# Kernel tuning notes

Measured on AMD Instinct MI355X. Metric: run time of the kernel, lower is better.

The kernel has to match this reference:

```python
import jax, jax.numpy as jnp
import numpy as np

N_GRAPHS = 32
NUM_NODES = 2848
N = N_GRAPHS * NUM_NODES  # 91136
E = 1_000_000
K = 3   # num_stacks
T = 5   # num_layers
HID = 32
EPS = 1e-5


def setup_inputs() -> dict:
    key = jax.random.key(0)
    ks = jax.random.split(key, 32)
    s = 0.1
    rn = lambda k, shp: (jax.random.normal(k, shp, jnp.float32) * s)
    inp = {
        "x": jax.random.normal(ks[0], (N, 2), jnp.float32),
        "edge_index": jax.random.randint(ks[1], (2, E), 0, N, dtype=jnp.int32).astype(jnp.int64),
        "weights": jax.random.uniform(ks[2], (E,), jnp.float32),
        "batch": (jnp.arange(N) // NUM_NODES).astype(jnp.int64),
        # ARMAConv1: 2 -> 32
        "iw1": rn(ks[3], (K, 2, HID)),
        "w1": rn(ks[4], (T - 1, K, HID, HID)),
        "rw1": rn(ks[5], (T, K, 2, HID)),
        "b1": rn(ks[6], (T, K, 1, HID)),
        "g1": jnp.ones((HID,), jnp.float32), "be1": jnp.zeros((HID,), jnp.float32),
        # ARMAConv2: 32 -> 32
        "iw2": rn(ks[7], (K, HID, HID)),
        "w2": rn(ks[8], (T - 1, K, HID, HID)),
        "rw2": rn(ks[9], (T, K, HID, HID)),
        "b2": rn(ks[10], (T, K, 1, HID)),
        "g2": jnp.ones((HID,), jnp.float32), "be2": jnp.zeros((HID,), jnp.float32),
        # ARMAConv3: 32 -> 1
        "iw3": rn(ks[11], (K, HID, 1)),
        "w3": rn(ks[12], (T - 1, K, 1, 1)),
        "rw3": rn(ks[13], (T, K, HID, 1)),
        "b3": rn(ks[14], (T, K, 1, 1)),
        "g3": jnp.ones((1,), jnp.float32), "be3": jnp.zeros((1,), jnp.float32),
        # classifier Linear(1, 1)
        "cw": rn(ks[15], (1, 1)),
        "cb": jnp.zeros((1,), jnp.float32),
    }
    return inp


def gcn_norm(row, col, w, n):
    # deg over targets, sym normalization, no self loops (PyG ARMAConv default)
    deg = jnp.zeros((n,), w.dtype).at[col].add(w)
    dis = jnp.where(deg > 0, jax.lax.rsqrt(jnp.where(deg > 0, deg, 1.0)), 0.0)
    return dis[row] * w * dis[col]


def arma_conv(x, row, col, norm, iw, w, rw, b):
    # x: [N, Fin]; returns [N, Fout] (mean over K stacks)
    out = None
    for t in range(T):
        if t == 0:
            h = jnp.einsum('nf,kfo->kno', x, iw)          # [K, N, Fout]
        else:
            h = jnp.einsum('kno,kop->knp', out, w[t - 1])
        msg = h[:, row, :] * norm[None, :, None]           # [K, E, Fout]
        agg = jnp.zeros_like(h).at[:, col, :].add(msg)     # scatter to targets
        out = jax.nn.relu(agg + jnp.einsum('nf,kfo->kno', x, rw[t]) + b[t])
    return out.mean(axis=0)


def batch_norm(x, g, b):
    m = x.mean(axis=0)
    v = x.var(axis=0)  # biased, as torch BatchNorm1d (training stats)
    return (x - m) * jax.lax.rsqrt(v + EPS) * g + b


def reference(x, edge_index, weights, batch,
              iw1, w1, rw1, b1, g1, be1,
              iw2, w2, rw2, b2, g2, be2,
              iw3, w3, rw3, b3, g3, be3,
              cw, cb):
    row, col = edge_index[0], edge_index[1]
    norm = gcn_norm(row, col, weights, N)

    h = arma_conv(x, row, col, norm, iw1, w1, rw1, b1)
    h = jax.nn.relu(batch_norm(h, g1, be1))
    h = arma_conv(h, row, col, norm, iw2, w2, rw2, b2)
    h = jax.nn.relu(batch_norm(h, g2, be2))
    h = arma_conv(h, row, col, norm, iw3, w3, rw3, b3)
    h = jax.nn.relu(batch_norm(h, g3, be3))  # [N, 1]

    # to_dense_batch: each graph has exactly NUM_NODES nodes -> reshape
    xd = h.reshape(N_GRAPHS, NUM_NODES, 1)
    logits_nodes = (xd @ cw.T + cb).squeeze(-1)   # [B, NUM_NODES]
    logits_graph = logits_nodes.max(axis=1)       # [B]
    return logits_nodes, logits_graph
```

## Files before the change

kernel.cpp:

```cpp
#include <hip/hip_runtime.h>
#include <hip/hip_fp16.h>

#define N_GRAPHS 32
#define NUM_NODES 2848
#define NTOT (N_GRAPHS * NUM_NODES)
#define NE 1000000
#define KS 3
#define TL 5
#define HID 32
#define EPSV 1e-5f
#define SCAN_B 256
#define NBLK (NTOT / SCAN_B)
#define NBINS 64
#define CNTN (NBINS * NBLK)
#define CNTB (CNTN / SCAN_B)
#define NT8 (NTOT * 8)
#define NB128 (NTOT / 128)
#define SRCMASK 0x1FFFFu

typedef unsigned uintx4 __attribute__((ext_vector_type(4)));


__device__ __forceinline__ float2 unpk(unsigned u) {
    return make_float2(__uint_as_float(u << 16), __uint_as_float(u & 0xffff0000u));
}
__device__ __forceinline__ unsigned bf16rn(float f) {
    unsigned x = __float_as_uint(f);
    return (x + 0x7fffu + ((x >> 16) & 1u)) >> 16;
}
__device__ __forceinline__ unsigned pk(float a, float b) {
    return bf16rn(a) | (bf16rn(b) << 16);
}
__device__ __forceinline__ float dec_nm(unsigned q) {
    return __half2float(__ushort_as_half((unsigned short)(q >> 17)));
}


__global__ void k_cnt(const int* __restrict__ col, int* __restrict__ indeg) {
    int e = blockIdx.x * blockDim.x + threadIdx.x;
    if (e < NE) atomicAdd(&indeg[col[e]], 1);
}

__global__ void k_lhist(const int* __restrict__ indeg, int* __restrict__ cnt) {
    __shared__ int h[NBINS];
    int t = threadIdx.x;
    if (t < NBINS) h[t] = 0;
    __syncthreads();
    int n = blockIdx.x * SCAN_B + t;
    atomicAdd(&h[min(indeg[n], NBINS - 1)], 1);
    __syncthreads();
    if (t < NBINS) cnt[t * NBLK + blockIdx.x] = h[t];
}

__global__ void k_scan1(const int* __restrict__ in, int* __restrict__ bsum) {
    __shared__ int s[SCAN_B];
    int i = blockIdx.x * SCAN_B + threadIdx.x;
    s[threadIdx.x] = in[i];
    __syncthreads();
    for (int st = SCAN_B / 2; st >= 1; st >>= 1) {
        if (threadIdx.x < st) s[threadIdx.x] += s[threadIdx.x + st];
        __syncthreads();
    }
    if (threadIdx.x == 0) bsum[blockIdx.x] = s[0];
}

__global__ void k_scan2(int* __restrict__ bsum, int n) {
    __shared__ int s[512];
    int t = threadIdx.x;
    int v = (t < n) ? bsum[t] : 0;
    s[t] = v;
    __syncthreads();
    for (int off = 1; off < 512; off <<= 1) {
        int a = (t >= off) ? s[t - off] : 0;
        __syncthreads();
        s[t] += a;
        __syncthreads();
    }
    if (t < n) bsum[t] = s[t] - v;
}

__global__ void k_scan3(const int* __restrict__ in, const int* __restrict__ bsum,
                        int* __restrict__ out, int sentIdx, int sentVal) {
    __shared__ int s[SCAN_B];
    int i = blockIdx.x * SCAN_B + threadIdx.x;
    int v = in[i];
    s[threadIdx.x] = v;
    __syncthreads();
    for (int off = 1; off < SCAN_B; off <<= 1) {
        int a = (threadIdx.x >= off) ? s[threadIdx.x - off] : 0;
        __syncthreads();
        s[threadIdx.x] += a;
        __syncthreads();
    }
    out[i] = bsum[blockIdx.x] + s[threadIdx.x] - v;
    if (i == 0 && sentIdx >= 0) out[sentIdx] = sentVal;
}

__global__ void k_rank(const int* __restrict__ indeg, const int* __restrict__ cnt,
                       int* __restrict__ perm, int* __restrict__ invperm,
                       int* __restrict__ indegp) {
    __shared__ int base[NBINS];
    __shared__ int cur[NBINS];
    int t = threadIdx.x;
    if (t < NBINS) { base[t] = cnt[t * NBLK + blockIdx.x]; cur[t] = 0; }
    __syncthreads();
    int n = blockIdx.x * SCAN_B + t;
    int dg = indeg[n];
    int b = min(dg, NBINS - 1);
    int pos = base[b] + atomicAdd(&cur[b], 1);
    perm[pos] = n;
    invperm[n] = pos;
    indegp[pos] = dg;
}

__global__ void k_xp(const float2* __restrict__ x, const int* __restrict__ perm,
                     float2* __restrict__ xp) {
    int i = blockIdx.x * blockDim.x + threadIdx.x;
    if (i < NTOT) xp[i] = x[perm[i]];
}

__global__ void k_fill(const int* __restrict__ row, const int* __restrict__ col,
                       const float* __restrict__ w, const int* __restrict__ invperm,
                       int* __restrict__ cursor, int2* __restrict__ adjtmp) {
    int e = blockIdx.x * blockDim.x + threadIdx.x;
    if (e < NE) {
        int pr = invperm[row[e]], pc = invperm[col[e]];
        int p = atomicAdd(&cursor[pc], 1);
        adjtmp[p] = make_int2(pr, __float_as_int(w[e]));
    }
}

__global__ void k_degdis(const int2* __restrict__ adjtmp, const int* __restrict__ offs,
                         float* __restrict__ disp) {
    int n = blockIdx.x * blockDim.x + threadIdx.x;
    if (n >= NTOT) return;
    int e0 = offs[n], e1 = offs[n + 1];
    float d = 0.f;
    for (int e = e0; e < e1; ++e) d += __int_as_float(adjtmp[e].y);
    disp[n] = (d > 0.f) ? rsqrtf(d) : 0.f;
}

__global__ void k_norm(const int2* __restrict__ adjtmp, const int* __restrict__ offs,
                       const float* __restrict__ disp, unsigned* __restrict__ adjc) {
    int n = blockIdx.x * blockDim.x + threadIdx.x;
    if (n >= NTOT) return;
    float dc = disp[n];
    int e0 = offs[n], e1 = offs[n + 1];
    for (int e = e0; e < e1; ++e) {
        int2 t = adjtmp[e];
        float nm = dc * __int_as_float(t.y) * disp[t.x];
        unsigned short hb = __half_as_ushort(__float2half(nm));
        adjc[e] = ((unsigned)hb << 17) | (unsigned)t.x;
    }
}


__global__ __launch_bounds__(256) void k_gath(
    const unsigned* __restrict__ SRC, const int* __restrict__ offs,
    const unsigned* __restrict__ adjc, unsigned* __restrict__ P) {
    int tid = threadIdx.x;
    int u = tid & 1;
    int nl = tid >> 1;
    int bid = blockIdx.x;
    int s = bid / NB128;
    int node = (bid - s * NB128) * 128 + nl;
    const uintx4* src = (const uintx4*)(SRC + (size_t)s * NT8);
    float a0 = 0.f, a1 = 0.f, a2 = 0.f, a3 = 0.f, a4 = 0.f, a5 = 0.f, a6 = 0.f, a7 = 0.f;
    int e0 = offs[node], e1 = offs[node + 1];
    int e = e0;
    for (; e + 4 <= e1; e += 4) {
        unsigned q0 = __builtin_nontemporal_load(adjc + e);
        unsigned q1 = __builtin_nontemporal_load(adjc + e + 1);
        unsigned q2 = __builtin_nontemporal_load(adjc + e + 2);
        unsigned q3 = __builtin_nontemporal_load(adjc + e + 3);
        uintx4 v0 = src[(q0 & SRCMASK) * 2 + u];
        uintx4 v1 = src[(q1 & SRCMASK) * 2 + u];
        uintx4 v2 = src[(q2 & SRCMASK) * 2 + u];
        uintx4 v3 = src[(q3 & SRCMASK) * 2 + u];
        float n0 = dec_nm(q0), n1 = dec_nm(q1), n2 = dec_nm(q2), n3 = dec_nm(q3);
        float2 t;
        t = unpk(v0.x); a0 += n0 * t.x; a1 += n0 * t.y;
        t = unpk(v0.y); a2 += n0 * t.x; a3 += n0 * t.y;
        t = unpk(v0.z); a4 += n0 * t.x; a5 += n0 * t.y;
        t = unpk(v0.w); a6 += n0 * t.x; a7 += n0 * t.y;
        t = unpk(v1.x); a0 += n1 * t.x; a1 += n1 * t.y;
        t = unpk(v1.y); a2 += n1 * t.x; a3 += n1 * t.y;
        t = unpk(v1.z); a4 += n1 * t.x; a5 += n1 * t.y;
        t = unpk(v1.w); a6 += n1 * t.x; a7 += n1 * t.y;
        t = unpk(v2.x); a0 += n2 * t.x; a1 += n2 * t.y;
        t = unpk(v2.y); a2 += n2 * t.x; a3 += n2 * t.y;
        t = unpk(v2.z); a4 += n2 * t.x; a5 += n2 * t.y;
        t = unpk(v2.w); a6 += n2 * t.x; a7 += n2 * t.y;
        t = unpk(v3.x); a0 += n3 * t.x; a1 += n3 * t.y;
        t = unpk(v3.y); a2 += n3 * t.x; a3 += n3 * t.y;
        t = unpk(v3.z); a4 += n3 * t.x; a5 += n3 * t.y;
        t = unpk(v3.w); a6 += n3 * t.x; a7 += n3 * t.y;
    }
    for (; e < e1; ++e) {
        unsigned q0 = __builtin_nontemporal_load(adjc + e);
        uintx4 v0 = src[(q0 & SRCMASK) * 2 + u];
        float n0 = dec_nm(q0);
        float2 t;
        t = unpk(v0.x); a0 += n0 * t.x; a1 += n0 * t.y;
        t = unpk(v0.y); a2 += n0 * t.x; a3 += n0 * t.y;
        t = unpk(v0.z); a4 += n0 * t.x; a5 += n0 * t.y;
        t = unpk(v0.w); a6 += n0 * t.x; a7 += n0 * t.y;
    }
    uintx4 o;
    o.x = pk(a0, a1); o.y = pk(a2, a3); o.z = pk(a4, a5); o.w = pk(a6, a7);
    __builtin_nontemporal_store(o, (uintx4*)(P + (size_t)s * NT8 + (size_t)node * 8) + u);
}


template<int FIN, bool PERK, bool LAST>
__global__ __launch_bounds__(256) void k_xform(
    const unsigned* __restrict__ P, const float* __restrict__ xin,
    const float* __restrict__ W, const float* __restrict__ rw,
    const float* __restrict__ bb, unsigned* __restrict__ OUTn,
    float* __restrict__ xm) {
    constexpr int SPK = PERK ? 3 : 1;
    constexpr int NSEC = PERK ? 6 : 2;
    constexpr int ND = 128;
    __shared__ unsigned sp[SPK][ND][17];
    __shared__ float xr[FIN == 32 ? ND : 1][FIN == 32 ? 33 : 1];
    int tid = threadIdx.x;
    int node0 = blockIdx.x * ND;
    for (int t4 = tid; t4 < NSEC * 256; t4 += 256) {
        int s = t4 >> 8, r = t4 & 255, n = r >> 1, u4 = (r & 1) * 4;
        uintx4 v = *(const uintx4*)(P + (size_t)s * NT8 + (size_t)(node0 + n) * 8 + u4);
        int kk = PERK ? (s >> 1) : 0;
        int base = (s & 1) * 8 + u4;
        sp[kk][n][base]     = v.x;
        sp[kk][n][base + 1] = v.y;
        sp[kk][n][base + 2] = v.z;
        sp[kk][n][base + 3] = v.w;
    }
    if constexpr (FIN == 32) {
        for (int t4 = tid; t4 < ND * 8; t4 += 256) {
            int n = t4 >> 3, j4 = (t4 & 7) * 4;
            float4 v = ((const float4*)xin)[(size_t)(node0 + n) * 8 + (t4 & 7)];
            xr[n][j4] = v.x; xr[n][j4 + 1] = v.y; xr[n][j4 + 2] = v.z; xr[n][j4 + 3] = v.w;
        }
    }
    __syncthreads();
    int f2 = tid & 15, nl = tid >> 4;
    int nbase = nl * 8;
    float2 xv2[8];
    if constexpr (FIN == 2) {
#pragma unroll
        for (int n = 0; n < 8; ++n) xv2[n] = ((const float2*)xin)[node0 + nbase + n];
    }
    float m0[8] = {}, m1[8] = {};
#pragma unroll
    for (int k = 0; k < KS; ++k) {
        constexpr int kkI = 0;
        const int kk = PERK ? k : kkI;
        float2 bv = ((const float2*)(bb + k * HID))[f2];
        float h0[8], h1[8];
#pragma unroll
        for (int n = 0; n < 8; ++n) { h0[n] = bv.x; h1[n] = bv.y; }
        const float2* W2 = (const float2*)(W + (size_t)k * HID * HID);
        const float2* R2 = (const float2*)(rw + (size_t)k * FIN * HID);
#pragma unroll 4
        for (int i2 = 0; i2 < 16; ++i2) {
            float2 wf0 = W2[(2 * i2) * 16 + f2];
            float2 wf1 = W2[(2 * i2 + 1) * 16 + f2];
            float2 rf0, rf1;
            if constexpr (FIN == 32) {
                rf0 = R2[(2 * i2) * 16 + f2];
                rf1 = R2[(2 * i2 + 1) * 16 + f2];
            }
#pragma unroll
            for (int n = 0; n < 8; ++n) {
                float2 sv = unpk(sp[kk][nbase + n][i2]);
                h0[n] += sv.x * wf0.x + sv.y * wf1.x;
                h1[n] += sv.x * wf0.y + sv.y * wf1.y;
                if constexpr (FIN == 32) {
                    float x0 = xr[nbase + n][2 * i2], x1 = xr[nbase + n][2 * i2 + 1];
                    h0[n] += x0 * rf0.x + x1 * rf1.x;
                    h1[n] += x0 * rf0.y + x1 * rf1.y;
                }
            }
        }
        if constexpr (FIN == 2) {
            float2 r0 = R2[0 * 16 + f2], r1 = R2[1 * 16 + f2];
#pragma unroll
            for (int n = 0; n < 8; ++n) {
                h0[n] += xv2[n].x * r0.x + xv2[n].y * r1.x;
                h1[n] += xv2[n].x * r0.y + xv2[n].y * r1.y;
            }
        }
#pragma unroll
        for (int n = 0; n < 8; ++n) {
            h0[n] = fmaxf(h0[n], 0.f);
            h1[n] = fmaxf(h1[n], 0.f);
            if constexpr (LAST) {
                m0[n] += h0[n]; m1[n] += h1[n];
            } else {
                OUTn[(size_t)(k * 2 + (f2 >> 3)) * NT8 +
                     (size_t)(node0 + nbase + n) * 8 + (f2 & 7)] = pk(h0[n], h1[n]);
            }
        }
    }
    if constexpr (LAST) {
#pragma unroll
        for (int n = 0; n < 8; ++n)
            ((float2*)xm)[(size_t)(node0 + nbase + n) * 16 + f2] =
                make_float2(m0[n] * (1.f / 3.f), m1[n] * (1.f / 3.f));
    }
}


__global__ void k_gath2(const float2* __restrict__ xp, const int* __restrict__ offs,
                        const unsigned* __restrict__ adjc, float2* __restrict__ pag) {
    int node = blockIdx.x * blockDim.x + threadIdx.x;
    if (node >= NTOT) return;
    float a0 = 0.f, a1 = 0.f;
    int e0 = offs[node], e1 = offs[node + 1];
    int e = e0;
    for (; e + 4 <= e1; e += 4) {
        unsigned q0 = __builtin_nontemporal_load(adjc + e);
        unsigned q1 = __builtin_nontemporal_load(adjc + e + 1);
        unsigned q2 = __builtin_nontemporal_load(adjc + e + 2);
        unsigned q3 = __builtin_nontemporal_load(adjc + e + 3);
        float2 x0 = xp[q0 & SRCMASK], x1 = xp[q1 & SRCMASK];
        float2 x2 = xp[q2 & SRCMASK], x3 = xp[q3 & SRCMASK];
        float n0 = dec_nm(q0), n1 = dec_nm(q1), n2 = dec_nm(q2), n3 = dec_nm(q3);
        a0 += n0 * x0.x + n1 * x1.x + n2 * x2.x + n3 * x3.x;
        a1 += n0 * x0.y + n1 * x1.y + n2 * x2.y + n3 * x3.y;
    }
    for (; e < e1; ++e) {
        unsigned q0 = __builtin_nontemporal_load(adjc + e);
        float2 xs = xp[q0 & SRCMASK];
        float nm = dec_nm(q0);
        a0 += nm * xs.x; a1 += nm * xs.y;
    }
    pag[node] = make_float2(a0, a1);
}

__global__ void k_x0(const float2* __restrict__ pag, const float2* __restrict__ xp,
                     const float* __restrict__ iw, const float* __restrict__ rw0,
                     const float* __restrict__ b0, unsigned* __restrict__ OUT) {
    int tid = blockIdx.x * blockDim.x + threadIdx.x;
    int f2 = tid & 15;
    int node = tid >> 4;
    float2 pv = pag[node];
    float2 xn = xp[node];
#pragma unroll
    for (int k = 0; k < KS; ++k) {
        const float2* iw2 = (const float2*)(iw + k * 2 * HID);
        const float2* rw2 = (const float2*)(rw0 + k * 2 * HID);
        float2 wi0 = iw2[0 * 16 + f2], wi1 = iw2[1 * 16 + f2];
        float2 wr0 = rw2[0 * 16 + f2], wr1 = rw2[1 * 16 + f2];
        float2 bv = ((const float2*)(b0 + k * HID))[f2];
        float o0 = fmaxf(pv.x * wi0.x + pv.y * wi1.x + xn.x * wr0.x + xn.y * wr1.x + bv.x, 0.f);
        float o1 = fmaxf(pv.x * wi0.y + pv.y * wi1.y + xn.x * wr0.y + xn.y * wr1.y + bv.y, 0.f);
        OUT[(size_t)(k * 2 + (f2 >> 3)) * NT8 + (size_t)node * 8 + (f2 & 7)] = pk(o0, o1);
    }
}


__global__ void k_init1(const float* __restrict__ x, const float* __restrict__ iw,
                        float4* __restrict__ H) {
    int n = blockIdx.x * blockDim.x + threadIdx.x;
    if (n >= NTOT) return;
    float a0 = 0.f, a1 = 0.f, a2 = 0.f;
#pragma unroll
    for (int i = 0; i < HID; ++i) {
        float xv = x[n * HID + i];
        a0 += xv * iw[0 * HID + i];
        a1 += xv * iw[1 * HID + i];
        a2 += xv * iw[2 * HID + i];
    }
    H[n] = make_float4(a0, a1, a2, 0.f);
}

template<bool LAST>
__global__ void k_prop1(const float4* __restrict__ H, const float* __restrict__ xin,
                        const float* __restrict__ rw_t, const float* __restrict__ b_t,
                        const float* __restrict__ W_t, const int* __restrict__ offs,
                        const unsigned* __restrict__ adjc, const int* __restrict__ perm,
                        float* __restrict__ outp) {
    int node = blockIdx.x * blockDim.x + threadIdx.x;
    if (node >= NTOT) return;
    float a0 = b_t[0], a1 = b_t[1], a2 = b_t[2];
#pragma unroll
    for (int i = 0; i < HID; ++i) {
        float xv = xin[node * HID + i];
        a0 += xv * rw_t[0 * HID + i];
        a1 += xv * rw_t[1 * HID + i];
        a2 += xv * rw_t[2 * HID + i];
    }
    int e0 = offs[node], e1 = offs[node + 1];
    int e = e0;
    for (; e + 4 <= e1; e += 4) {
        unsigned q0 = __builtin_nontemporal_load(adjc + e);
        unsigned q1 = __builtin_nontemporal_load(adjc + e + 1);
        unsigned q2 = __builtin_nontemporal_load(adjc + e + 2);
        unsigned q3 = __builtin_nontemporal_load(adjc + e + 3);
        float4 h0 = H[q0 & SRCMASK], h1 = H[q1 & SRCMASK];
        float4 h2 = H[q2 & SRCMASK], h3 = H[q3 & SRCMASK];
        float n0 = dec_nm(q0), n1 = dec_nm(q1), n2 = dec_nm(q2), n3 = dec_nm(q3);
        a0 += n0 * h0.x; a1 += n0 * h0.y; a2 += n0 * h0.z;
        a0 += n1 * h1.x; a1 += n1 * h1.y; a2 += n1 * h1.z;
        a0 += n2 * h2.x; a1 += n2 * h2.y; a2 += n2 * h2.z;
        a0 += n3 * h3.x; a1 += n3 * h3.y; a2 += n3 * h3.z;
    }
    for (; e < e1; ++e) {
        unsigned q0 = __builtin_nontemporal_load(adjc + e);
        float4 h = H[q0 & SRCMASK];
        float nm = dec_nm(q0);
        a0 += nm * h.x; a1 += nm * h.y; a2 += nm * h.z;
    }
    a0 = fmaxf(a0, 0.f); a1 = fmaxf(a1, 0.f); a2 = fmaxf(a2, 0.f);
    if constexpr (LAST) {
        outp[perm[node]] = (a0 + a1 + a2) * (1.f / 3.f);
    } else {
        ((float4*)outp)[node] = make_float4(a0 * W_t[0], a1 * W_t[1], a2 * W_t[2], 0.f);
    }
}


__global__ void k_bnstats(const float* __restrict__ x, float* __restrict__ stats, int F) {
    __shared__ float s1[256];
    __shared__ float s2[256];
    int tid = threadIdx.x;
    int gid = blockIdx.x * blockDim.x + tid;
    int stride = gridDim.x * blockDim.x;
    int total = NTOT * F;
    float a = 0.f, b = 0.f;
    for (int i = gid; i < total; i += stride) {
        float v = x[i];
        a += v;
        b += v * v;
    }
    s1[tid] = a; s2[tid] = b;
    __syncthreads();
    for (int s = 128; s >= F; s >>= 1) {
        if (tid < s) { s1[tid] += s1[tid + s]; s2[tid] += s2[tid + s]; }
        __syncthreads();
    }
    if (tid < F) {
        atomicAdd(&stats[tid], s1[tid]);
        atomicAdd(&stats[F + tid], s2[tid]);
    }
}

__global__ void k_bnapply32(float* __restrict__ x, const float* __restrict__ stats,
                            const float* __restrict__ g, const float* __restrict__ be,
                            unsigned* __restrict__ xbf) {
    int tid = blockIdx.x * blockDim.x + threadIdx.x;
    int f2 = tid & 15;
    int node = tid >> 4;
    int f0 = 2 * f2, f1 = f0 + 1;
    float mm0 = stats[f0] * (1.f / NTOT);
    float vv0 = stats[HID + f0] * (1.f / NTOT) - mm0 * mm0;
    float mm1 = stats[f1] * (1.f / NTOT);
    float vv1 = stats[HID + f1] * (1.f / NTOT) - mm1 * mm1;
    float y0 = fmaxf((x[(size_t)node * 32 + f0] - mm0) * rsqrtf(vv0 + EPSV) * g[f0] + be[f0], 0.f);
    float y1 = fmaxf((x[(size_t)node * 32 + f1] - mm1) * rsqrtf(vv1 + EPSV) * g[f1] + be[f1], 0.f);
    x[(size_t)node * 32 + f0] = y0;
    x[(size_t)node * 32 + f1] = y1;
    if (xbf) xbf[(size_t)(f2 >> 3) * NT8 + (size_t)node * 8 + (f2 & 7)] = pk(y0, y1);
}

__global__ void k_bnapply1(float* __restrict__ x, const float* __restrict__ stats,
                           const float* __restrict__ g, const float* __restrict__ be) {
    int i = blockIdx.x * blockDim.x + threadIdx.x;
    if (i >= NTOT) return;
    float m = stats[0] * (1.f / NTOT);
    float v = stats[1] * (1.f / NTOT) - m * m;
    float y = (x[i] - m) * rsqrtf(v + EPSV) * g[0] + be[0];
    x[i] = fmaxf(y, 0.f);
}


__global__ void k_final(const float* __restrict__ h, const float* __restrict__ cw,
                        const float* __restrict__ cb, float* __restrict__ out) {
    __shared__ float smax[256];
    int g = blockIdx.x;
    float cwv = cw[0], cbv = cb[0];
    float mx = -INFINITY;
    for (int i = threadIdx.x; i < NUM_NODES; i += blockDim.x) {
        int nidx = g * NUM_NODES + i;
        float v = h[nidx] * cwv + cbv;
        out[nidx] = v;
        mx = fmaxf(mx, v);
    }
    smax[threadIdx.x] = mx;
    __syncthreads();
    for (int s = 128; s >= 1; s >>= 1) {
        if (threadIdx.x < s) smax[threadIdx.x] = fmaxf(smax[threadIdx.x], smax[threadIdx.x + s]);
        __syncthreads();
    }
    if (threadIdx.x == 0) out[NTOT + g] = smax[0];
}


extern "C" void kernel_launch(void* const* d_in, const int* in_sizes, int n_in,
                              void* d_out, int out_size, void* d_ws, size_t ws_size,
                              hipStream_t stream) {
    const float* x   = (const float*)d_in[0];
    const int*   ei  = (const int*)d_in[1];
    const int*   row = ei;
    const int*   col = ei + NE;
    const float* wts = (const float*)d_in[2];
    const float* iw1 = (const float*)d_in[4];
    const float* w1  = (const float*)d_in[5];
    const float* rw1 = (const float*)d_in[6];
    const float* b1  = (const float*)d_in[7];
    const float* g1  = (const float*)d_in[8];
    const float* be1 = (const float*)d_in[9];
    const float* iw2 = (const float*)d_in[10];
    const float* w2  = (const float*)d_in[11];
    const float* rw2 = (const float*)d_in[12];
    const float* b2  = (const float*)d_in[13];
    const float* g2  = (const float*)d_in[14];
    const float* be2 = (const float*)d_in[15];
    const float* iw3 = (const float*)d_in[16];
    const float* w3  = (const float*)d_in[17];
    const float* rw3 = (const float*)d_in[18];
    const float* b3  = (const float*)d_in[19];
    const float* g3  = (const float*)d_in[20];
    const float* be3 = (const float*)d_in[21];
    const float* cw  = (const float*)d_in[22];
    const float* cb  = (const float*)d_in[23];
    float* out = (float*)d_out;

    char* p = (char*)d_ws;
    auto alloc = [&](size_t bytes) {
        char* r = p;
        p += (bytes + 255) & ~(size_t)255;
        return r;
    };
    int*      indeg  = (int*)alloc((size_t)NTOT * 4);
    int*      cnt    = (int*)alloc((size_t)CNTN * 4);
    char*     zend   = p;
    int*      bsum   = (int*)alloc((size_t)NBLK * 4);
    int*      offs   = (int*)alloc((size_t)(NTOT + 1) * 4);
    int*      cursor = (int*)alloc((size_t)NTOT * 4);
    int*      perm   = (int*)alloc((size_t)NTOT * 4);
    int*      invperm= (int*)alloc((size_t)NTOT * 4);
    int*      indegp = (int*)alloc((size_t)NTOT * 4);
    float*    disp   = (float*)alloc((size_t)NTOT * 4);
    int2*     adjtmp = (int2*)alloc((size_t)NE * 8);
    unsigned* adjc   = (unsigned*)alloc((size_t)NE * 4);
    unsigned* OUTA   = (unsigned*)alloc((size_t)6 * NT8 * 4);
    unsigned* OUTB   = (unsigned*)alloc((size_t)6 * NT8 * 4);
    unsigned* P      = (unsigned*)alloc((size_t)6 * NT8 * 4);
    unsigned* xplane = (unsigned*)alloc((size_t)2 * NT8 * 4);
    float2*   xp     = (float2*)alloc((size_t)NTOT * 8);
    float2*   pag    = (float2*)alloc((size_t)NTOT * 8);
    float*    xa     = (float*)alloc((size_t)NTOT * HID * 4);
    float*    xb     = (float*)alloc((size_t)NTOT * HID * 4);
    float*    xc     = (float*)alloc((size_t)NTOT * 4);
    float*    stats  = (float*)alloc(3 * 2 * HID * 4);
    if ((size_t)(p - (char*)d_ws) > ws_size) return;

    const int tb = 256;
    const int ebl = (NE + tb - 1) / tb;
    const int nbl = NTOT / tb;
    const int g16 = NTOT * 16 / tb;

    hipMemsetAsync(indeg, 0, (size_t)(zend - (char*)indeg), stream);
    hipMemsetAsync(stats, 0, (size_t)3 * 2 * HID * 4, stream);

    k_cnt<<<ebl, tb, 0, stream>>>(col, indeg);
    k_lhist<<<NBLK, SCAN_B, 0, stream>>>(indeg, cnt);
    k_scan1<<<CNTB, SCAN_B, 0, stream>>>(cnt, bsum);
    k_scan2<<<1, 512, 0, stream>>>(bsum, CNTB);
    k_scan3<<<CNTB, SCAN_B, 0, stream>>>(cnt, bsum, cnt, -1, 0);
    k_rank<<<NBLK, SCAN_B, 0, stream>>>(indeg, cnt, perm, invperm, indegp);
    k_xp<<<nbl, tb, 0, stream>>>((const float2*)x, perm, xp);
    k_scan1<<<NBLK, SCAN_B, 0, stream>>>(indegp, bsum);
    k_scan2<<<1, 512, 0, stream>>>(bsum, NBLK);
    k_scan3<<<NBLK, SCAN_B, 0, stream>>>(indegp, bsum, offs, NTOT, NE);
    hipMemcpyAsync(cursor, offs, (size_t)NTOT * 4, hipMemcpyDeviceToDevice, stream);
    k_fill<<<ebl, tb, 0, stream>>>(row, col, wts, invperm, cursor, adjtmp);
    k_degdis<<<nbl, tb, 0, stream>>>(adjtmp, offs, disp);
    k_norm<<<nbl, tb, 0, stream>>>(adjtmp, offs, disp, adjc);

    {
        k_gath2<<<nbl, tb, 0, stream>>>(xp, offs, adjc, pag);
        k_x0<<<g16, tb, 0, stream>>>(pag, xp, iw1, rw1, b1, OUTA);
        unsigned* Hc = OUTA; unsigned* Hn = OUTB;
        for (int t = 1; t < TL - 1; ++t) {
            k_gath<<<6 * NB128, tb, 0, stream>>>(Hc, offs, adjc, P);
            k_xform<2, true, false><<<NB128, tb, 0, stream>>>(
                P, (const float*)xp, w1 + (size_t)(t - 1) * KS * HID * HID,
                rw1 + (size_t)t * KS * 2 * HID, b1 + (size_t)t * KS * HID, Hn, nullptr);
            unsigned* tmp = Hc; Hc = Hn; Hn = tmp;
        }
        k_gath<<<6 * NB128, tb, 0, stream>>>(Hc, offs, adjc, P);
        k_xform<2, true, true><<<NB128, tb, 0, stream>>>(
            P, (const float*)xp, w1 + (size_t)(TL - 2) * KS * HID * HID,
            rw1 + (size_t)(TL - 1) * KS * 2 * HID, b1 + (size_t)(TL - 1) * KS * HID,
            nullptr, xa);
        k_bnstats<<<256, tb, 0, stream>>>(xa, stats, HID);
        k_bnapply32<<<g16, tb, 0, stream>>>(xa, stats, g1, be1, xplane);
    }
    {
        k_gath<<<2 * NB128, tb, 0, stream>>>(xplane, offs, adjc, P);
        k_xform<32, false, false><<<NB128, tb, 0, stream>>>(
            P, xa, iw2, rw2, b2, OUTA, nullptr);
        unsigned* Hc = OUTA; unsigned* Hn = OUTB;
        for (int t = 1; t < TL - 1; ++t) {
            k_gath<<<6 * NB128, tb, 0, stream>>>(Hc, offs, adjc, P);
            k_xform<32, true, false><<<NB128, tb, 0, stream>>>(
                P, xa, w2 + (size_t)(t - 1) * KS * HID * HID,
                rw2 + (size_t)t * KS * HID * HID, b2 + (size_t)t * KS * HID, Hn, nullptr);
            unsigned* tmp = Hc; Hc = Hn; Hn = tmp;
        }
        k_gath<<<6 * NB128, tb, 0, stream>>>(Hc, offs, adjc, P);
        k_xform<32, true, true><<<NB128, tb, 0, stream>>>(
            P, xa, w2 + (size_t)(TL - 2) * KS * HID * HID,
            rw2 + (size_t)(TL - 1) * KS * HID * HID, b2 + (size_t)(TL - 1) * KS * HID,
            nullptr, xb);
        k_bnstats<<<256, tb, 0, stream>>>(xb, stats + 2 * HID, HID);
        k_bnapply32<<<g16, tb, 0, stream>>>(xb, stats + 2 * HID, g2, be2, nullptr);
    }
    {
        float4* HAf = (float4*)OUTA;
        float4* HBf = (float4*)OUTB;
        k_init1<<<nbl, tb, 0, stream>>>(xb, iw3, HAf);
        const float4* Hc = HAf; float4* Hn = HBf;
        for (int t = 0; t < TL - 1; ++t) {
            k_prop1<false><<<nbl, tb, 0, stream>>>(
                Hc, xb, rw3 + (size_t)t * KS * HID, b3 + (size_t)t * KS,
                w3 + (size_t)t * KS, offs, adjc, perm, (float*)Hn);
            const float4* tmp = Hc; Hc = Hn; Hn = (float4*)tmp;
        }
        k_prop1<true><<<nbl, tb, 0, stream>>>(
            Hc, xb, rw3 + (size_t)(TL - 1) * KS * HID, b3 + (size_t)(TL - 1) * KS,
            nullptr, offs, adjc, perm, xc);
        k_bnstats<<<256, tb, 0, stream>>>(xc, stats + 4 * HID, 1);
        k_bnapply1<<<nbl, tb, 0, stream>>>(xc, stats + 4 * HID, g3, be3);
    }

    k_final<<<N_GRAPHS, 256, 0, stream>>>(xc, cw, cb, out);
}
```

Before: 1.171 ms.

## Make gather kernel persistent with XCC-affine atomic work queue per feature section

Replaces the one-block-per-(section, node chunk) gather launch with a fixed grid of persistent blocks. Each block pulls node chunks from per-section atomic counters, starting with a section chosen from its XCC id. The goal is for each XCC to work mostly on one source section so its gathered rows stay in that XCC's L2, cutting cross-die traffic and misses. The cost is an atomic plus two barriers per chunk, and XCC-to-section imbalance falls back to stealing from other sections. The counters are zeroed once per call by the existing memset and get a fresh slot for each launch.

```diff
diff --git a/kernel.cpp b/kernel.cpp
--- a/kernel.cpp
+++ b/kernel.cpp
@@ -17,6 +17,7 @@
 #define NT8 (NTOT * 8)
 #define NB128 (NTOT / 128)
 #define SRCMASK 0x1FFFFu
+#define QSLOTS 16
 
 typedef unsigned uintx4 __attribute__((ext_vector_type(4)));
 
@@ -157,58 +158,77 @@
 
 __global__ __launch_bounds__(256) void k_gath(
     const unsigned* __restrict__ SRC, const int* __restrict__ offs,
-    const unsigned* __restrict__ adjc, unsigned* __restrict__ P) {
+    const unsigned* __restrict__ adjc, unsigned* __restrict__ P,
+    int* __restrict__ qcur, int nsec) {
+    __shared__ int sc_s, sc_c;
+    unsigned xcc = 0;
+    asm volatile("s_getreg_b32 %0, hwreg(HW_REG_XCC_ID)" : "=s"(xcc));
+    int prim = (int)(xcc & 7) % nsec;
     int tid = threadIdx.x;
     int u = tid & 1;
     int nl = tid >> 1;
-    int bid = blockIdx.x;
-    int s = bid / NB128;
-    int node = (bid - s * NB128) * 128 + nl;
-    const uintx4* src = (const uintx4*)(SRC + (size_t)s * NT8);
-    float a0 = 0.f, a1 = 0.f, a2 = 0.f, a3 = 0.f, a4 = 0.f, a5 = 0.f, a6 = 0.f, a7 = 0.f;
-    int e0 = offs[node], e1 = offs[node + 1];
-    int e = e0;
-    for (; e + 4 <= e1; e += 4) {
-        unsigned q0 = __builtin_nontemporal_load(adjc + e);
-        unsigned q1 = __builtin_nontemporal_load(adjc + e + 1);
-        unsigned q2 = __builtin_nontemporal_load(adjc + e + 2);
-        unsigned q3 = __builtin_nontemporal_load(adjc + e + 3);
-        uintx4 v0 = src[(q0 & SRCMASK) * 2 + u];
-        uintx4 v1 = src[(q1 & SRCMASK) * 2 + u];
-        uintx4 v2 = src[(q2 & SRCMASK) * 2 + u];
-        uintx4 v3 = src[(q3 & SRCMASK) * 2 + u];
-        float n0 = dec_nm(q0), n1 = dec_nm(q1), n2 = dec_nm(q2), n3 = dec_nm(q3);
-        float2 t;
-        t = unpk(v0.x); a0 += n0 * t.x; a1 += n0 * t.y;
-        t = unpk(v0.y); a2 += n0 * t.x; a3 += n0 * t.y;
-        t = unpk(v0.z); a4 += n0 * t.x; a5 += n0 * t.y;
-        t = unpk(v0.w); a6 += n0 * t.x; a7 += n0 * t.y;
-        t = unpk(v1.x); a0 += n1 * t.x; a1 += n1 * t.y;
-        t = unpk(v1.y); a2 += n1 * t.x; a3 += n1 * t.y;
-        t = unpk(v1.z); a4 += n1 * t.x; a5 += n1 * t.y;
-        t = unpk(v1.w); a6 += n1 * t.x; a7 += n1 * t.y;
-        t = unpk(v2.x); a0 += n2 * t.x; a1 += n2 * t.y;
-        t = unpk(v2.y); a2 += n2 * t.x; a3 += n2 * t.y;
-        t = unpk(v2.z); a4 += n2 * t.x; a5 += n2 * t.y;
-        t = unpk(v2.w); a6 += n2 * t.x; a7 += n2 * t.y;
-        t = unpk(v3.x); a0 += n3 * t.x; a1 += n3 * t.y;
-        t = unpk(v3.y); a2 += n3 * t.x; a3 += n3 * t.y;
-        t = unpk(v3.z); a4 += n3 * t.x; a5 += n3 * t.y;
-        t = unpk(v3.w); a6 += n3 * t.x; a7 += n3 * t.y;
-    }
-    for (; e < e1; ++e) {
-        unsigned q0 = __builtin_nontemporal_load(adjc + e);
-        uintx4 v0 = src[(q0 & SRCMASK) * 2 + u];
-        float n0 = dec_nm(q0);
-        float2 t;
-        t = unpk(v0.x); a0 += n0 * t.x; a1 += n0 * t.y;
-        t = unpk(v0.y); a2 += n0 * t.x; a3 += n0 * t.y;
-        t = unpk(v0.z); a4 += n0 * t.x; a5 += n0 * t.y;
-        t = unpk(v0.w); a6 += n0 * t.x; a7 += n0 * t.y;
-    }
-    uintx4 o;
-    o.x = pk(a0, a1); o.y = pk(a2, a3); o.z = pk(a4, a5); o.w = pk(a6, a7);
-    __builtin_nontemporal_store(o, (uintx4*)(P + (size_t)s * NT8 + (size_t)node * 8) + u);
+    for (;;) {
+        if (tid == 0) {
+            int s = -1, c = -1;
+            for (int t = 0; t < nsec; ++t) {
+                int ss = prim + t; if (ss >= nsec) ss -= nsec;
+                int cc = atomicAdd(&qcur[ss], 1);
+                if (cc < NB128) { s = ss; c = cc; break; }
+            }
+            sc_s = s; sc_c = c;
+        }
+        __syncthreads();
+        int s = sc_s, c = sc_c;
+        __syncthreads();
+        if (s < 0) return;
+        int node = c * 128 + nl;
+        const uintx4* src = (const uintx4*)(SRC + (size_t)s * NT8);
+        float a0 = 0.f, a1 = 0.f, a2 = 0.f, a3 = 0.f;
+        float a4 = 0.f, a5 = 0.f, a6 = 0.f, a7 = 0.f;
+        int e0 = offs[node], e1 = offs[node + 1];
+        int e = e0;
+        for (; e + 4 <= e1; e += 4) {
+            unsigned q0 = __builtin_nontemporal_load(adjc + e);
+            unsigned q1 = __builtin_nontemporal_load(adjc + e + 1);
+            unsigned q2 = __builtin_nontemporal_load(adjc + e + 2);
+            unsigned q3 = __builtin_nontemporal_load(adjc + e + 3);
+            uintx4 v0 = src[(q0 & SRCMASK) * 2 + u];
+            uintx4 v1 = src[(q1 & SRCMASK) * 2 + u];
+            uintx4 v2 = src[(q2 & SRCMASK) * 2 + u];
+            uintx4 v3 = src[(q3 & SRCMASK) * 2 + u];
+            float n0 = dec_nm(q0), n1 = dec_nm(q1), n2 = dec_nm(q2), n3 = dec_nm(q3);
+            float2 t;
+            t = unpk(v0.x); a0 += n0 * t.x; a1 += n0 * t.y;
+            t = unpk(v0.y); a2 += n0 * t.x; a3 += n0 * t.y;
+            t = unpk(v0.z); a4 += n0 * t.x; a5 += n0 * t.y;
+            t = unpk(v0.w); a6 += n0 * t.x; a7 += n0 * t.y;
+            t = unpk(v1.x); a0 += n1 * t.x; a1 += n1 * t.y;
+            t = unpk(v1.y); a2 += n1 * t.x; a3 += n1 * t.y;
+            t = unpk(v1.z); a4 += n1 * t.x; a5 += n1 * t.y;
+            t = unpk(v1.w); a6 += n1 * t.x; a7 += n1 * t.y;
+            t = unpk(v2.x); a0 += n2 * t.x; a1 += n2 * t.y;
+            t = unpk(v2.y); a2 += n2 * t.x; a3 += n2 * t.y;
+            t = unpk(v2.z); a4 += n2 * t.x; a5 += n2 * t.y;
+            t = unpk(v2.w); a6 += n2 * t.x; a7 += n2 * t.y;
+            t = unpk(v3.x); a0 += n3 * t.x; a1 += n3 * t.y;
+            t = unpk(v3.y); a2 += n3 * t.x; a3 += n3 * t.y;
+            t = unpk(v3.z); a4 += n3 * t.x; a5 += n3 * t.y;
+            t = unpk(v3.w); a6 += n3 * t.x; a7 += n3 * t.y;
+        }
+        for (; e < e1; ++e) {
+            unsigned q0 = __builtin_nontemporal_load(adjc + e);
+            uintx4 v0 = src[(q0 & SRCMASK) * 2 + u];
+            float n0 = dec_nm(q0);
+            float2 t;
+            t = unpk(v0.x); a0 += n0 * t.x; a1 += n0 * t.y;
+            t = unpk(v0.y); a2 += n0 * t.x; a3 += n0 * t.y;
+            t = unpk(v0.z); a4 += n0 * t.x; a5 += n0 * t.y;
+            t = unpk(v0.w); a6 += n0 * t.x; a7 += n0 * t.y;
+        }
+        uintx4 o;
+        o.x = pk(a0, a1); o.y = pk(a2, a3); o.z = pk(a4, a5); o.w = pk(a6, a7);
+        __builtin_nontemporal_store(o, (uintx4*)(P + (size_t)s * NT8 + (size_t)node * 8) + u);
+    }
 }
 
 
@@ -535,6 +555,7 @@
     };
     int*      indeg  = (int*)alloc((size_t)NTOT * 4);
     int*      cnt    = (int*)alloc((size_t)CNTN * 4);
+    int*      qcur   = (int*)alloc((size_t)QSLOTS * 8 * 4);
     char*     zend   = p;
     int*      bsum   = (int*)alloc((size_t)NBLK * 4);
     int*      offs   = (int*)alloc((size_t)(NTOT + 1) * 4);
@@ -561,6 +582,8 @@
     const int ebl = (NE + tb - 1) / tb;
     const int nbl = NTOT / tb;
     const int g16 = NTOT * 16 / tb;
+    const int gpers = 2048;
+    int qslot = 0;
 
     hipMemsetAsync(indeg, 0, (size_t)(zend - (char*)indeg), stream);
     hipMemsetAsync(stats, 0, (size_t)3 * 2 * HID * 4, stream);
@@ -585,13 +608,13 @@
         k_x0<<<g16, tb, 0, stream>>>(pag, xp, iw1, rw1, b1, OUTA);
         unsigned* Hc = OUTA; unsigned* Hn = OUTB;
         for (int t = 1; t < TL - 1; ++t) {
-            k_gath<<<6 * NB128, tb, 0, stream>>>(Hc, offs, adjc, P);
+            k_gath<<<gpers, tb, 0, stream>>>(Hc, offs, adjc, P, qcur + 8 * qslot++, 6);
             k_xform<2, true, false><<<NB128, tb, 0, stream>>>(
                 P, (const float*)xp, w1 + (size_t)(t - 1) * KS * HID * HID,
                 rw1 + (size_t)t * KS * 2 * HID, b1 + (size_t)t * KS * HID, Hn, nullptr);
             unsigned* tmp = Hc; Hc = Hn; Hn = tmp;
         }
-        k_gath<<<6 * NB128, tb, 0, stream>>>(Hc, offs, adjc, P);
+        k_gath<<<gpers, tb, 0, stream>>>(Hc, offs, adjc, P, qcur + 8 * qslot++, 6);
         k_xform<2, true, true><<<NB128, tb, 0, stream>>>(
             P, (const float*)xp, w1 + (size_t)(TL - 2) * KS * HID * HID,
             rw1 + (size_t)(TL - 1) * KS * 2 * HID, b1 + (size_t)(TL - 1) * KS * HID,
@@ -600,18 +623,18 @@
         k_bnapply32<<<g16, tb, 0, stream>>>(xa, stats, g1, be1, xplane);
     }
     {
-        k_gath<<<2 * NB128, tb, 0, stream>>>(xplane, offs, adjc, P);
+        k_gath<<<gpers, tb, 0, stream>>>(xplane, offs, adjc, P, qcur + 8 * qslot++, 2);
         k_xform<32, false, false><<<NB128, tb, 0, stream>>>(
             P, xa, iw2, rw2, b2, OUTA, nullptr);
         unsigned* Hc = OUTA; unsigned* Hn = OUTB;
         for (int t = 1; t < TL - 1; ++t) {
-            k_gath<<<6 * NB128, tb, 0, stream>>>(Hc, offs, adjc, P);
+            k_gath<<<gpers, tb, 0, stream>>>(Hc, offs, adjc, P, qcur + 8 * qslot++, 6);
             k_xform<32, true, false><<<NB128, tb, 0, stream>>>(
                 P, xa, w2 + (size_t)(t - 1) * KS * HID * HID,
                 rw2 + (size_t)t * KS * HID * HID, b2 + (size_t)t * KS * HID, Hn, nullptr);
             unsigned* tmp = Hc; Hc = Hn; Hn = tmp;
         }
-        k_gath<<<6 * NB128, tb, 0, stream>>>(Hc, offs, adjc, P);
+        k_gath<<<gpers, tb, 0, stream>>>(Hc, offs, adjc, P, qcur + 8 * qslot++, 6);
         k_xform<32, true, true><<<NB128, tb, 0, stream>>>(
             P, xa, w2 + (size_t)(TL - 2) * KS * HID * HID,
             rw2 + (size_t)(TL - 1) * KS * HID * HID, b2 + (size_t)(TL - 1) * KS * HID,
```

Result: slower. 2.366 ms (+102.1%).

## Pack edge weights into compressed adjacency and precompute layer-3 root terms

Applied to the files above, without the earlier changes.

The edge fill now writes the 32-bit packed adjacency directly, storing the raw edge weight as fp16 alongside the source index, and the degree and normalization kernels read and rewrite that packed array in place instead of an 8-byte int2 temporary. In the third ARMA layer, a new kernel reads each node's 32-wide features once and computes the initial projection plus all five root-weight projections, storing them in a per-layer float4 buffer. The propagation kernels then load a single float4 instead of re-reading 32 floats per step. This trades fp16 rounding of the raw weights in the degree sum (a precision risk) and an extra buffer for less memory traffic.

```diff
diff --git a/kernel.cpp b/kernel.cpp
--- a/kernel.cpp
+++ b/kernel.cpp
@@ -121,36 +121,37 @@
 
 __global__ void k_fill(const int* __restrict__ row, const int* __restrict__ col,
                        const float* __restrict__ w, const int* __restrict__ invperm,
-                       int* __restrict__ cursor, int2* __restrict__ adjtmp) {
+                       int* __restrict__ cursor, unsigned* __restrict__ adjc) {
     int e = blockIdx.x * blockDim.x + threadIdx.x;
     if (e < NE) {
         int pr = invperm[row[e]], pc = invperm[col[e]];
         int p = atomicAdd(&cursor[pc], 1);
-        adjtmp[p] = make_int2(pr, __float_as_int(w[e]));
-    }
-}
-
-__global__ void k_degdis(const int2* __restrict__ adjtmp, const int* __restrict__ offs,
+        unsigned short hb = __half_as_ushort(__float2half(w[e]));
+        adjc[p] = ((unsigned)hb << 17) | (unsigned)pr;
+    }
+}
+
+__global__ void k_degdis(const unsigned* __restrict__ adjc, const int* __restrict__ offs,
                          float* __restrict__ disp) {
     int n = blockIdx.x * blockDim.x + threadIdx.x;
     if (n >= NTOT) return;
     int e0 = offs[n], e1 = offs[n + 1];
     float d = 0.f;
-    for (int e = e0; e < e1; ++e) d += __int_as_float(adjtmp[e].y);
+    for (int e = e0; e < e1; ++e) d += dec_nm(adjc[e]);
     disp[n] = (d > 0.f) ? rsqrtf(d) : 0.f;
 }
 
-__global__ void k_norm(const int2* __restrict__ adjtmp, const int* __restrict__ offs,
-                       const float* __restrict__ disp, unsigned* __restrict__ adjc) {
+__global__ void k_norm(unsigned* __restrict__ adjc, const int* __restrict__ offs,
+                       const float* __restrict__ disp) {
     int n = blockIdx.x * blockDim.x + threadIdx.x;
     if (n >= NTOT) return;
     float dc = disp[n];
     int e0 = offs[n], e1 = offs[n + 1];
     for (int e = e0; e < e1; ++e) {
-        int2 t = adjtmp[e];
-        float nm = dc * __int_as_float(t.y) * disp[t.x];
+        unsigned q = adjc[e];
+        float nm = dc * dec_nm(q) * disp[q & SRCMASK];
         unsigned short hb = __half_as_ushort(__float2half(nm));
-        adjc[e] = ((unsigned)hb << 17) | (unsigned)t.x;
+        adjc[e] = ((unsigned)hb << 17) | (q & SRCMASK);
     }
 }
 
@@ -360,37 +361,50 @@
 }
 
 
-__global__ void k_init1(const float* __restrict__ x, const float* __restrict__ iw,
-                        float4* __restrict__ H) {
+__global__ void k_rec3(const float* __restrict__ xb, const float* __restrict__ iw3,
+                       const float* __restrict__ rw3, const float* __restrict__ b3,
+                       float4* __restrict__ H0, float4* __restrict__ RT) {
     int n = blockIdx.x * blockDim.x + threadIdx.x;
     if (n >= NTOT) return;
-    float a0 = 0.f, a1 = 0.f, a2 = 0.f;
-#pragma unroll
-    for (int i = 0; i < HID; ++i) {
-        float xv = x[n * HID + i];
-        a0 += xv * iw[0 * HID + i];
-        a1 += xv * iw[1 * HID + i];
-        a2 += xv * iw[2 * HID + i];
-    }
-    H[n] = make_float4(a0, a1, a2, 0.f);
+    float xr[HID];
+#pragma unroll
+    for (int j = 0; j < 8; ++j) {
+        float4 v = ((const float4*)xb)[(size_t)n * 8 + j];
+        xr[4 * j] = v.x; xr[4 * j + 1] = v.y; xr[4 * j + 2] = v.z; xr[4 * j + 3] = v.w;
+    }
+    {
+        float a0 = 0.f, a1 = 0.f, a2 = 0.f;
+#pragma unroll
+        for (int i = 0; i < HID; ++i) {
+            a0 += xr[i] * iw3[0 * HID + i];
+            a1 += xr[i] * iw3[1 * HID + i];
+            a2 += xr[i] * iw3[2 * HID + i];
+        }
+        H0[n] = make_float4(a0, a1, a2, 0.f);
+    }
+#pragma unroll
+    for (int t = 0; t < TL; ++t) {
+        float a0 = b3[t * KS + 0], a1 = b3[t * KS + 1], a2 = b3[t * KS + 2];
+        const float* r = rw3 + (size_t)t * KS * HID;
+#pragma unroll
+        for (int i = 0; i < HID; ++i) {
+            a0 += xr[i] * r[0 * HID + i];
+            a1 += xr[i] * r[1 * HID + i];
+            a2 += xr[i] * r[2 * HID + i];
+        }
+        RT[(size_t)t * NTOT + n] = make_float4(a0, a1, a2, 0.f);
+    }
 }
 
 template<bool LAST>
-__global__ void k_prop1(const float4* __restrict__ H, const float* __restrict__ xin,
-                        const float* __restrict__ rw_t, const float* __restrict__ b_t,
+__global__ void k_prop1(const float4* __restrict__ H, const float4* __restrict__ RT,
                         const float* __restrict__ W_t, const int* __restrict__ offs,
                         const unsigned* __restrict__ adjc, const int* __restrict__ perm,
                         float* __restrict__ outp) {
     int node = blockIdx.x * blockDim.x + threadIdx.x;
     if (node >= NTOT) return;
-    float a0 = b_t[0], a1 = b_t[1], a2 = b_t[2];
-#pragma unroll
-    for (int i = 0; i < HID; ++i) {
-        float xv = xin[node * HID + i];
-        a0 += xv * rw_t[0 * HID + i];
-        a1 += xv * rw_t[1 * HID + i];
-        a2 += xv * rw_t[2 * HID + i];
-    }
+    float4 rt = RT[node];
+    float a0 = rt.x, a1 = rt.y, a2 = rt.z;
     int e0 = offs[node], e1 = offs[node + 1];
     int e = e0;
     for (; e + 4 <= e1; e += 4) {
@@ -543,7 +557,6 @@
     int*      invperm= (int*)alloc((size_t)NTOT * 4);
     int*      indegp = (int*)alloc((size_t)NTOT * 4);
     float*    disp   = (float*)alloc((size_t)NTOT * 4);
-    int2*     adjtmp = (int2*)alloc((size_t)NE * 8);
     unsigned* adjc   = (unsigned*)alloc((size_t)NE * 4);
     unsigned* OUTA   = (unsigned*)alloc((size_t)6 * NT8 * 4);
     unsigned* OUTB   = (unsigned*)alloc((size_t)6 * NT8 * 4);
@@ -554,6 +567,7 @@
     float*    xa     = (float*)alloc((size_t)NTOT * HID * 4);
     float*    xb     = (float*)alloc((size_t)NTOT * HID * 4);
     float*    xc     = (float*)alloc((size_t)NTOT * 4);
+    float4*   RT     = (float4*)alloc((size_t)TL * NTOT * 16);
     float*    stats  = (float*)alloc(3 * 2 * HID * 4);
     if ((size_t)(p - (char*)d_ws) > ws_size) return;
 
@@ -576,9 +590,9 @@
     k_scan2<<<1, 512, 0, stream>>>(bsum, NBLK);
     k_scan3<<<NBLK, SCAN_B, 0, stream>>>(indegp, bsum, offs, NTOT, NE);
     hipMemcpyAsync(cursor, offs, (size_t)NTOT * 4, hipMemcpyDeviceToDevice, stream);
-    k_fill<<<ebl, tb, 0, stream>>>(row, col, wts, invperm, cursor, adjtmp);
-    k_degdis<<<nbl, tb, 0, stream>>>(adjtmp, offs, disp);
-    k_norm<<<nbl, tb, 0, stream>>>(adjtmp, offs, disp, adjc);
+    k_fill<<<ebl, tb, 0, stream>>>(row, col, wts, invperm, cursor, adjc);
+    k_degdis<<<nbl, tb, 0, stream>>>(adjc, offs, disp);
+    k_norm<<<nbl, tb, 0, stream>>>(adjc, offs, disp);
 
     {
         k_gath2<<<nbl, tb, 0, stream>>>(xp, offs, adjc, pag);
@@ -622,17 +636,15 @@
     {
         float4* HAf = (float4*)OUTA;
         float4* HBf = (float4*)OUTB;
-        k_init1<<<nbl, tb, 0, stream>>>(xb, iw3, HAf);
+        k_rec3<<<nbl, tb, 0, stream>>>(xb, iw3, rw3, b3, HAf, RT);
         const float4* Hc = HAf; float4* Hn = HBf;
         for (int t = 0; t < TL - 1; ++t) {
             k_prop1<false><<<nbl, tb, 0, stream>>>(
-                Hc, xb, rw3 + (size_t)t * KS * HID, b3 + (size_t)t * KS,
-                w3 + (size_t)t * KS, offs, adjc, perm, (float*)Hn);
+                Hc, RT + (size_t)t * NTOT, w3 + (size_t)t * KS, offs, adjc, perm, (float*)Hn);
             const float4* tmp = Hc; Hc = Hn; Hn = (float4*)tmp;
         }
         k_prop1<true><<<nbl, tb, 0, stream>>>(
-            Hc, xb, rw3 + (size_t)(TL - 1) * KS * HID, b3 + (size_t)(TL - 1) * KS,
-            nullptr, offs, adjc, perm, xc);
+            Hc, RT + (size_t)(TL - 1) * NTOT, nullptr, offs, adjc, perm, xc);
         k_bnstats<<<256, tb, 0, stream>>>(xc, stats + 4 * HID, 1);
         k_bnapply1<<<nbl, tb, 0, stream>>>(xc, stats + 4 * HID, g3, be3);
     }
```

Result: no change. 1.166 ms (-0.4%).
